# Performance work log

Measured on AMD Instinct MI355X. Metric: run time of the kernel, lower is better.

The kernel has to match this reference:

```python
import jax, jax.numpy as jnp
import numpy as np

N_CLASS = 100
DECAY = 0.3
THRESHOLD = 0.9


def _weighted_centroid(feature, y, prev_centroid):
    # labels/logits from per-class scores
    labels = jnp.argmax(y, axis=1)                      # [n] int
    logits = jnp.max(y, axis=1)                         # [n]
    # per-class counts, clamped at 1
    counts = jax.ops.segment_sum(jnp.ones_like(logits), labels, num_segments=N_CLASS)
    counts = jnp.maximum(counts, 1.0)                   # [n_class]
    # threshold-masked confidence weights
    w = jnp.where(logits > THRESHOLD, logits, 0.0)      # [n]
    # confidence-weighted scatter-add of features by class label
    sums = jax.ops.segment_sum(w[:, None] * feature, labels, num_segments=N_CLASS)  # [n_class, d]
    cur = sums / counts[:, None]
    return (1.0 - DECAY) * prev_centroid + DECAY * cur


def setup_inputs() -> dict:
    key = jax.random.key(0)
    ks = jax.random.split(key, 6)
    n, d = 131072, 256
    return {
        "s_feature": jax.random.normal(ks[0], (n, d), dtype=jnp.float32),
        "t_feature": jax.random.normal(ks[1], (n, d), dtype=jnp.float32),
        "y_s": jax.random.normal(ks[2], (n, N_CLASS), dtype=jnp.float32),
        "y_t": jax.random.normal(ks[3], (n, N_CLASS), dtype=jnp.float32),
        "s_centroid": jax.random.normal(ks[4], (N_CLASS, d), dtype=jnp.float32),
        "t_centroid": jax.random.normal(ks[5], (N_CLASS, d), dtype=jnp.float32),
    }


def reference(s_feature, t_feature, y_s, y_t, s_centroid, t_centroid):
    s_c = _weighted_centroid(s_feature, y_s, s_centroid)
    t_c = _weighted_centroid(t_feature, y_t, t_centroid)
    # MSELoss: mean over all elements
    semantic_loss = jnp.mean((s_c - t_c) ** 2)
    return semantic_loss
```

## Files before the change

### kernel.cpp

```cpp
#include <hip/hip_runtime.h>

#define N_CLASS 100
#define D 256
#define DECAYF 0.3f
#define KEEPF 0.7f
#define THRESH 0.9f
#define RB 64
#define BB 256
#define NSLICE 8

__global__ void argmax_kernel(const float* __restrict__ yS, const float* __restrict__ yT,
                              int* __restrict__ lbl, float* __restrict__ w,
                              int* __restrict__ cntPart, int n, int NB) {
    const int t = blockIdx.y;
    const float* __restrict__ y = t ? yT : yS;

    __shared__ float ly[RB * N_CLASS];
    __shared__ int hist[N_CLASS];
    const int tid = threadIdx.x;
    if (tid < N_CLASS) hist[tid] = 0;

    const float4* __restrict__ src = (const float4*)(y + (size_t)blockIdx.x * (RB * N_CLASS));
    for (int i = tid; i < RB * N_CLASS / 4; i += 256)
        ((float4*)ly)[i] = src[i];
    __syncthreads();

    const int row = tid >> 2;
    const int q = tid & 3;
    const int base = row * N_CLASS + q * 25;

    float best = -3.4e38f;
    int bi = 0;
    #pragma unroll
    for (int k = 0; k < 25; ++k) {
        float v = ly[base + k];
        if (v > best) { best = v; bi = q * 25 + k; }
    }
    #pragma unroll
    for (int off = 1; off <= 2; off <<= 1) {
        float ov = __shfl_xor(best, off, 64);
        int   oi = __shfl_xor(bi, off, 64);
        if (ov > best || (ov == best && oi < bi)) { best = ov; bi = oi; }
    }
    if (q == 0) {
        const int grow = blockIdx.x * RB + row;
        lbl[(size_t)t * n + grow] = bi;
        w[(size_t)t * n + grow] = (best > THRESH) ? best : 0.0f;
        atomicAdd(&hist[bi], 1);
    }
    __syncthreads();
    if (tid < N_CLASS) cntPart[(t * N_CLASS + tid) * NB + blockIdx.x] = hist[tid];
}

__global__ void scan_kernel(const int* __restrict__ cntPart, int* __restrict__ relOff,
                            int* __restrict__ totals, int NB) {
    const int tc = blockIdx.x;
    const int* __restrict__ src = cntPart + (size_t)tc * NB;
    int* __restrict__ dst = relOff + (size_t)tc * NB;
    const int tid = threadIdx.x;
    const int EPT = NB / 256;

    int v[8];
    int s = 0;
    for (int k = 0; k < EPT; ++k) { v[k] = src[tid * EPT + k]; s += v[k]; }

    __shared__ int ls[256];
    ls[tid] = s;
    __syncthreads();
    for (int off = 1; off < 256; off <<= 1) {
        int x = (tid >= off) ? ls[tid - off] : 0;
        __syncthreads();
        ls[tid] += x;
        __syncthreads();
    }
    int run = (tid ? ls[tid - 1] : 0);
    for (int k = 0; k < EPT; ++k) { dst[tid * EPT + k] = run; run += v[k]; }
    if (tid == 255) totals[tc] = run;
}

__global__ void base_kernel(const int* __restrict__ totals, int* __restrict__ classBase) {
    __shared__ int ls[2][128];
    const int t = threadIdx.x >> 7;
    const int c = threadIdx.x & 127;
    int v = (c < N_CLASS) ? totals[t * N_CLASS + c] : 0;
    ls[t][c] = v;
    __syncthreads();
    for (int off = 1; off < 128; off <<= 1) {
        int x = (c >= off) ? ls[t][c - off] : 0;
        __syncthreads();
        ls[t][c] += x;
        __syncthreads();
    }
    if (c < N_CLASS) classBase[t * N_CLASS + c] = ls[t][c] - v;
}

__global__ void bucket_kernel(const int* __restrict__ lbl, const float* __restrict__ w,
                              const int* __restrict__ relOff, const int* __restrict__ classBase,
                              int2* __restrict__ sPair, int n, int NB) {
    const int t = blockIdx.y;
    const int b = blockIdx.x;
    __shared__ int cursor[N_CLASS];
    const int tid = threadIdx.x;
    if (tid < N_CLASS)
        cursor[tid] = classBase[t * N_CLASS + tid] +
                      relOff[(size_t)(t * N_CLASS + tid) * NB + 4 * b];
    __syncthreads();
    const int row = b * BB + tid;
    const int l = lbl[(size_t)t * n + row];
    const float wt = w[(size_t)t * n + row];
    const int pos = atomicAdd(&cursor[l], 1);
    sPair[(size_t)t * n + pos] = make_int2(row, __float_as_int(wt));
}

__global__ void __launch_bounds__(256, 4)
gather_kernel(const float* __restrict__ fS, const float* __restrict__ fT,
              const int2* __restrict__ sPair,
              const int* __restrict__ totals, const int* __restrict__ classBase,
              float* __restrict__ partial, int n) {
    const int c = blockIdx.x;
    const int s = blockIdx.y;
    const int t = blockIdx.z;
    const float* __restrict__ f = t ? fT : fS;
    const int2* __restrict__ sp = sPair + (size_t)t * n;

    const int start = classBase[t * N_CLASS + c];
    const int cnt = totals[t * N_CLASS + c];
    const int per = (cnt + NSLICE - 1) / NSLICE;
    int lo = start + s * per;
    int hi = start + cnt;
    if (lo + per < hi) hi = lo + per;
    if (hi < lo) hi = lo;

    const int tid = threadIdx.x;
    const int lane = tid & 63;
    const int wv = tid >> 6;

    float4 acc = {0.f, 0.f, 0.f, 0.f};
    const int span = hi - lo;
    const int m = span / 32;

    int2 p[8];
    if (m > 0) {
        const int i0 = lo + wv * 8;
        #pragma unroll
        for (int j = 0; j < 8; ++j) p[j] = sp[i0 + j];
    }
    for (int kk = 0; kk < m; ++kk) {
        float4 v[8];
        #pragma unroll
        for (int j = 0; j < 8; ++j)
            v[j] = *(const float4*)(f + (size_t)p[j].x * D + lane * 4);
        int2 np[8];
        if (kk + 1 < m) {
            const int i1 = lo + (kk + 1) * 32 + wv * 8;
            #pragma unroll
            for (int j = 0; j < 8; ++j) np[j] = sp[i1 + j];
        }
        #pragma unroll
        for (int j = 0; j < 8; ++j) {
            const float wt = __int_as_float(p[j].y);
            acc.x += wt * v[j].x; acc.y += wt * v[j].y;
            acc.z += wt * v[j].z; acc.w += wt * v[j].w;
        }
        #pragma unroll
        for (int j = 0; j < 8; ++j) p[j] = np[j];
    }
    for (int r = lo + m * 32 + wv; r < hi; r += 4) {
        const int2 pr = sp[r];
        const float wt = __int_as_float(pr.y);
        const float4 v = *(const float4*)(f + (size_t)pr.x * D + lane * 4);
        acc.x += wt * v.x; acc.y += wt * v.y; acc.z += wt * v.z; acc.w += wt * v.w;
    }

    __shared__ float4 red[4][64];
    red[wv][lane] = acc;
    __syncthreads();
    if (wv == 0) {
        float4 a0 = red[0][lane], a1 = red[1][lane], a2 = red[2][lane], a3 = red[3][lane];
        float4 r4;
        r4.x = a0.x + a1.x + a2.x + a3.x;
        r4.y = a0.y + a1.y + a2.y + a3.y;
        r4.z = a0.z + a1.z + a2.z + a3.z;
        r4.w = a0.w + a1.w + a2.w + a3.w;
        *(float4*)(partial + (size_t)((t * N_CLASS + c) * NSLICE + s) * D + lane * 4) = r4;
    }
}

__global__ void finalize_kernel(const float* __restrict__ partial, const int* __restrict__ totals,
                                const float* __restrict__ cS, const float* __restrict__ cT,
                                float* __restrict__ out) {
    const int c = blockIdx.x;
    const int j = threadIdx.x;

    float sS = 0.f, sT = 0.f;
    #pragma unroll
    for (int s = 0; s < NSLICE; ++s) {
        sS += partial[(size_t)((0 * N_CLASS + c) * NSLICE + s) * D + j];
        sT += partial[(size_t)((1 * N_CLASS + c) * NSLICE + s) * D + j];
    }
    const float cntS = fmaxf((float)totals[c], 1.0f);
    const float cntT = fmaxf((float)totals[N_CLASS + c], 1.0f);
    const float a = KEEPF * cS[c * D + j] + DECAYF * sS / cntS;
    const float b = KEEPF * cT[c * D + j] + DECAYF * sT / cntT;
    const float d = a - b;
    float val = d * d;

    #pragma unroll
    for (int off = 32; off; off >>= 1) val += __shfl_xor(val, off, 64);
    __shared__ float red[4];
    if ((j & 63) == 0) red[j >> 6] = val;
    __syncthreads();
    if (j == 0)
        unsafeAtomicAdd(out, (red[0] + red[1] + red[2] + red[3]) * (1.0f / (N_CLASS * D)));
}

extern "C" void kernel_launch(void* const* d_in, const int* in_sizes, int n_in,
                              void* d_out, int out_size, void* d_ws, size_t ws_size,
                              hipStream_t stream) {
    const float* s_feature = (const float*)d_in[0];
    const float* t_feature = (const float*)d_in[1];
    const float* y_s = (const float*)d_in[2];
    const float* y_t = (const float*)d_in[3];
    const float* s_centroid = (const float*)d_in[4];
    const float* t_centroid = (const float*)d_in[5];
    float* out = (float*)d_out;

    const int n = in_sizes[0] / D;
    const int NB = n / RB;

    int* lbl = (int*)d_ws;
    float* w = (float*)(lbl + 2 * n);
    int* cntPart = (int*)(w + 2 * n);
    int* relOff = cntPart + 2 * N_CLASS * NB;
    int* totals = relOff + 2 * N_CLASS * NB;
    int* classBase = totals + 256;
    int2* sPair = (int2*)(classBase + 256);
    float* partial = (float*)(sPair + 2 * n);

    hipMemsetAsync(out, 0, sizeof(float), stream);

    argmax_kernel<<<dim3(NB, 2), 256, 0, stream>>>(y_s, y_t, lbl, w, cntPart, n, NB);
    scan_kernel<<<2 * N_CLASS, 256, 0, stream>>>(cntPart, relOff, totals, NB);
    base_kernel<<<1, 256, 0, stream>>>(totals, classBase);
    bucket_kernel<<<dim3(n / BB, 2), BB, 0, stream>>>(lbl, w, relOff, classBase, sPair, n, NB);
    gather_kernel<<<dim3(N_CLASS, NSLICE, 2), 256, 0, stream>>>(s_feature, t_feature, sPair,
                                                                totals, classBase, partial, n);
    finalize_kernel<<<N_CLASS, 256, 0, stream>>>(partial, totals, s_centroid, t_centroid, out);
}
```

Before: 369.6 us.

## Fuse argmax and class scatter into one kernel with LDS atomic accumulation

Replaces the six-kernel pipeline (argmax, count scan, base offsets, bucket sort, gather, finalize) with two kernels. In the new main kernel each wave reads one row's scores and features per step, prefetching the next row, and finds the argmax with wave shuffles. It then atomically adds the weighted features into a per-block 100x256 accumulator held in shared memory. A second kernel sums the per-block partials, applies the centroid update and reduces the MSE. This drops the intermediate label and pair arrays, the scans and the scattered gather, reading each input once and streaming. The costs are LDS atomic contention, 100KB of shared memory per block that limits occupancy, and extra partial-buffer traffic for the cross-block reduction.

Result: slower. 626.6 us (+69.5%).

```diff
diff --git a/kernel.cpp b/kernel.cpp
--- a/kernel.cpp
+++ b/kernel.cpp
@@ -5,213 +5,126 @@
 #define DECAYF 0.3f
 #define KEEPF 0.7f
 #define THRESH 0.9f
-#define RB 64
-#define BB 256
-#define NSLICE 8
+#define ACC_SZ (N_CLASS * D)
 
-__global__ void argmax_kernel(const float* __restrict__ yS, const float* __restrict__ yT,
-                              int* __restrict__ lbl, float* __restrict__ w,
-                              int* __restrict__ cntPart, int n, int NB) {
+__global__ void __launch_bounds__(1024)
+mega_kernel(const float* __restrict__ fS, const float* __restrict__ fT,
+            const float* __restrict__ yS, const float* __restrict__ yT,
+            float* __restrict__ partial, int* __restrict__ counts,
+            int n, int B) {
     const int t = blockIdx.y;
+    const float* __restrict__ f = t ? fT : fS;
     const float* __restrict__ y = t ? yT : yS;
 
-    __shared__ float ly[RB * N_CLASS];
-    __shared__ int hist[N_CLASS];
+    __shared__ __align__(16) float acc[ACC_SZ];
+    __shared__ int cnt[N_CLASS];
+
     const int tid = threadIdx.x;
-    if (tid < N_CLASS) hist[tid] = 0;
-
-    const float4* __restrict__ src = (const float4*)(y + (size_t)blockIdx.x * (RB * N_CLASS));
-    for (int i = tid; i < RB * N_CLASS / 4; i += 256)
-        ((float4*)ly)[i] = src[i];
+    for (int i = tid; i < ACC_SZ; i += 1024) acc[i] = 0.f;
+    if (tid < N_CLASS) cnt[tid] = 0;
     __syncthreads();
 
-    const int row = tid >> 2;
-    const int q = tid & 3;
-    const int base = row * N_CLASS + q * 25;
+    const int lane = tid & 63;
+    const int wv = tid >> 6;
+    const int RPB = n / B;
+    const int RPW = RPB >> 4;
+    const int base = blockIdx.x * RPB + wv * RPW;
 
-    float best = -3.4e38f;
-    int bi = 0;
-    #pragma unroll
-    for (int k = 0; k < 25; ++k) {
-        float v = ly[base + k];
-        if (v > best) { best = v; bi = q * 25 + k; }
+    float4 yq = make_float4(0.f, 0.f, 0.f, 0.f);
+    if (lane < N_CLASS / 4)
+        yq = ((const float4*)(y + (size_t)base * N_CLASS))[lane];
+    float4 fv = *(const float4*)(f + (size_t)base * D + lane * 4);
+
+    for (int i = 0; i < RPW; ++i) {
+        float4 nyq = make_float4(0.f, 0.f, 0.f, 0.f);
+        float4 nfv = make_float4(0.f, 0.f, 0.f, 0.f);
+        if (i + 1 < RPW) {
+            const int nrow = base + i + 1;
+            if (lane < N_CLASS / 4)
+                nyq = ((const float4*)(y + (size_t)nrow * N_CLASS))[lane];
+            nfv = *(const float4*)(f + (size_t)nrow * D + lane * 4);
+        }
+
+        float best = -3.4e38f;
+        int bi = 0x7fffffff;
+        if (lane < N_CLASS / 4) {
+            const int c0 = lane * 4;
+            if (yq.x > best) { best = yq.x; bi = c0;     }
+            if (yq.y > best) { best = yq.y; bi = c0 + 1; }
+            if (yq.z > best) { best = yq.z; bi = c0 + 2; }
+            if (yq.w > best) { best = yq.w; bi = c0 + 3; }
+        }
+        #pragma unroll
+        for (int off = 1; off < 64; off <<= 1) {
+            const float ov = __shfl_xor(best, off, 64);
+            const int   oi = __shfl_xor(bi, off, 64);
+            if (ov > best || (ov == best && oi < bi)) { best = ov; bi = oi; }
+        }
+        const float wt = (best > THRESH) ? best : 0.f;
+        if (lane == 0) atomicAdd(&cnt[bi], 1);
+
+        float* a = acc + bi * D + lane;
+        atomicAdd(a,       wt * fv.x);
+        atomicAdd(a + 64,  wt * fv.y);
+        atomicAdd(a + 128, wt * fv.z);
+        atomicAdd(a + 192, wt * fv.w);
+
+        yq = nyq; fv = nfv;
+    }
+    __syncthreads();
+
+    float* outP = partial + ((size_t)t * B + blockIdx.x) * ACC_SZ;
+    for (int i = tid; i < ACC_SZ / 4; i += 1024)
+        ((float4*)outP)[i] = ((const float4*)acc)[i];
+    if (tid < N_CLASS) atomicAdd(&counts[t * N_CLASS + tid], cnt[tid]);
+}
+
+__global__ void __launch_bounds__(512)
+reduce_kernel(const float* __restrict__ partial, const int* __restrict__ counts,
+              const float* __restrict__ cS, const float* __restrict__ cT,
+              float* __restrict__ out, int B) {
+    const int c = blockIdx.x;
+    const int tid = threadIdx.x;
+    const int t = tid >> 8;
+    const int j = tid & 255;
+
+    const float* __restrict__ p = partial + (size_t)t * B * ACC_SZ + c * D + j;
+    float s = 0.f;
+    int b = 0;
+    for (; b + 4 <= B; b += 4) {
+        const float a0 = p[(size_t)(b + 0) * ACC_SZ];
+        const float a1 = p[(size_t)(b + 1) * ACC_SZ];
+        const float a2 = p[(size_t)(b + 2) * ACC_SZ];
+        const float a3 = p[(size_t)(b + 3) * ACC_SZ];
+        s += a0 + a1 + a2 + a3;
+    }
+    for (; b < B; ++b) s += p[(size_t)b * ACC_SZ];
+
+    const float cf = fmaxf((float)counts[t * N_CLASS + c], 1.0f);
+    const int c_log = 4 * (j & 63) + (j >> 6);
+    const float* __restrict__ cX = t ? cT : cS;
+    const float upd = KEEPF * cX[c * D + c_log] + DECAYF * s / cf;
+
+    __shared__ float u[2][D];
+    u[t][j] = upd;
+    __syncthreads();
+
+    float val = 0.f;
+    if (t == 0) {
+        const float d = u[0][j] - u[1][j];
+        val = d * d;
     }
     #pragma unroll
-    for (int off = 1; off <= 2; off <<= 1) {
-        float ov = __shfl_xor(best, off, 64);
-        int   oi = __shfl_xor(bi, off, 64);
-        if (ov > best || (ov == best && oi < bi)) { best = ov; bi = oi; }
+    for (int off = 32; off; off >>= 1) val += __shfl_xor(val, off, 64);
+    __shared__ float red[8];
+    if ((tid & 63) == 0) red[tid >> 6] = val;
+    __syncthreads();
+    if (tid == 0) {
+        float tot = 0.f;
+        #pragma unroll
+        for (int k = 0; k < 8; ++k) tot += red[k];
+        unsafeAtomicAdd(out, tot * (1.0f / (N_CLASS * D)));
     }
-    if (q == 0) {
-        const int grow = blockIdx.x * RB + row;
-        lbl[(size_t)t * n + grow] = bi;
-        w[(size_t)t * n + grow] = (best > THRESH) ? best : 0.0f;
-        atomicAdd(&hist[bi], 1);
-    }
-    __syncthreads();
-    if (tid < N_CLASS) cntPart[(t * N_CLASS + tid) * NB + blockIdx.x] = hist[tid];
-}
-
-__global__ void scan_kernel(const int* __restrict__ cntPart, int* __restrict__ relOff,
-                            int* __restrict__ totals, int NB) {
-    const int tc = blockIdx.x;
-    const int* __restrict__ src = cntPart + (size_t)tc * NB;
-    int* __restrict__ dst = relOff + (size_t)tc * NB;
-    const int tid = threadIdx.x;
-    const int EPT = NB / 256;
-
-    int v[8];
-    int s = 0;
-    for (int k = 0; k < EPT; ++k) { v[k] = src[tid * EPT + k]; s += v[k]; }
-
-    __shared__ int ls[256];
-    ls[tid] = s;
-    __syncthreads();
-    for (int off = 1; off < 256; off <<= 1) {
-        int x = (tid >= off) ? ls[tid - off] : 0;
-        __syncthreads();
-        ls[tid] += x;
-        __syncthreads();
-    }
-    int run = (tid ? ls[tid - 1] : 0);
-    for (int k = 0; k < EPT; ++k) { dst[tid * EPT + k] = run; run += v[k]; }
-    if (tid == 255) totals[tc] = run;
-}
-
-__global__ void base_kernel(const int* __restrict__ totals, int* __restrict__ classBase) {
-    __shared__ int ls[2][128];
-    const int t = threadIdx.x >> 7;
-    const int c = threadIdx.x & 127;
-    int v = (c < N_CLASS) ? totals[t * N_CLASS + c] : 0;
-    ls[t][c] = v;
-    __syncthreads();
-    for (int off = 1; off < 128; off <<= 1) {
-        int x = (c >= off) ? ls[t][c - off] : 0;
-        __syncthreads();
-        ls[t][c] += x;
-        __syncthreads();
-    }
-    if (c < N_CLASS) classBase[t * N_CLASS + c] = ls[t][c] - v;
-}
-
-__global__ void bucket_kernel(const int* __restrict__ lbl, const float* __restrict__ w,
-                              const int* __restrict__ relOff, const int* __restrict__ classBase,
-                              int2* __restrict__ sPair, int n, int NB) {
-    const int t = blockIdx.y;
-    const int b = blockIdx.x;
-    __shared__ int cursor[N_CLASS];
-    const int tid = threadIdx.x;
-    if (tid < N_CLASS)
-        cursor[tid] = classBase[t * N_CLASS + tid] +
-                      relOff[(size_t)(t * N_CLASS + tid) * NB + 4 * b];
-    __syncthreads();
-    const int row = b * BB + tid;
-    const int l = lbl[(size_t)t * n + row];
-    const float wt = w[(size_t)t * n + row];
-    const int pos = atomicAdd(&cursor[l], 1);
-    sPair[(size_t)t * n + pos] = make_int2(row, __float_as_int(wt));
-}
-
-__global__ void __launch_bounds__(256, 4)
-gather_kernel(const float* __restrict__ fS, const float* __restrict__ fT,
-              const int2* __restrict__ sPair,
-              const int* __restrict__ totals, const int* __restrict__ classBase,
-              float* __restrict__ partial, int n) {
-    const int c = blockIdx.x;
-    const int s = blockIdx.y;
-    const int t = blockIdx.z;
-    const float* __restrict__ f = t ? fT : fS;
-    const int2* __restrict__ sp = sPair + (size_t)t * n;
-
-    const int start = classBase[t * N_CLASS + c];
-    const int cnt = totals[t * N_CLASS + c];
-    const int per = (cnt + NSLICE - 1) / NSLICE;
-    int lo = start + s * per;
-    int hi = start + cnt;
-    if (lo + per < hi) hi = lo + per;
-    if (hi < lo) hi = lo;
-
-    const int tid = threadIdx.x;
-    const int lane = tid & 63;
-    const int wv = tid >> 6;
-
-    float4 acc = {0.f, 0.f, 0.f, 0.f};
-    const int span = hi - lo;
-    const int m = span / 32;
-
-    int2 p[8];
-    if (m > 0) {
-        const int i0 = lo + wv * 8;
-        #pragma unroll
-        for (int j = 0; j < 8; ++j) p[j] = sp[i0 + j];
-    }
-    for (int kk = 0; kk < m; ++kk) {
-        float4 v[8];
-        #pragma unroll
-        for (int j = 0; j < 8; ++j)
-            v[j] = *(const float4*)(f + (size_t)p[j].x * D + lane * 4);
-        int2 np[8];
-        if (kk + 1 < m) {
-            const int i1 = lo + (kk + 1) * 32 + wv * 8;
-            #pragma unroll
-            for (int j = 0; j < 8; ++j) np[j] = sp[i1 + j];
-        }
-        #pragma unroll
-        for (int j = 0; j < 8; ++j) {
-            const float wt = __int_as_float(p[j].y);
-            acc.x += wt * v[j].x; acc.y += wt * v[j].y;
-            acc.z += wt * v[j].z; acc.w += wt * v[j].w;
-        }
-        #pragma unroll
-        for (int j = 0; j < 8; ++j) p[j] = np[j];
-    }
-    for (int r = lo + m * 32 + wv; r < hi; r += 4) {
-        const int2 pr = sp[r];
-        const float wt = __int_as_float(pr.y);
-        const float4 v = *(const float4*)(f + (size_t)pr.x * D + lane * 4);
-        acc.x += wt * v.x; acc.y += wt * v.y; acc.z += wt * v.z; acc.w += wt * v.w;
-    }
-
-    __shared__ float4 red[4][64];
-    red[wv][lane] = acc;
-    __syncthreads();
-    if (wv == 0) {
-        float4 a0 = red[0][lane], a1 = red[1][lane], a2 = red[2][lane], a3 = red[3][lane];
-        float4 r4;
-        r4.x = a0.x + a1.x + a2.x + a3.x;
-        r4.y = a0.y + a1.y + a2.y + a3.y;
-        r4.z = a0.z + a1.z + a2.z + a3.z;
-        r4.w = a0.w + a1.w + a2.w + a3.w;
-        *(float4*)(partial + (size_t)((t * N_CLASS + c) * NSLICE + s) * D + lane * 4) = r4;
-    }
-}
-
-__global__ void finalize_kernel(const float* __restrict__ partial, const int* __restrict__ totals,
-                                const float* __restrict__ cS, const float* __restrict__ cT,
-                                float* __restrict__ out) {
-    const int c = blockIdx.x;
-    const int j = threadIdx.x;
-
-    float sS = 0.f, sT = 0.f;
-    #pragma unroll
-    for (int s = 0; s < NSLICE; ++s) {
-        sS += partial[(size_t)((0 * N_CLASS + c) * NSLICE + s) * D + j];
-        sT += partial[(size_t)((1 * N_CLASS + c) * NSLICE + s) * D + j];
-    }
-    const float cntS = fmaxf((float)totals[c], 1.0f);
-    const float cntT = fmaxf((float)totals[N_CLASS + c], 1.0f);
-    const float a = KEEPF * cS[c * D + j] + DECAYF * sS / cntS;
-    const float b = KEEPF * cT[c * D + j] + DECAYF * sT / cntT;
-    const float d = a - b;
-    float val = d * d;
-
-    #pragma unroll
-    for (int off = 32; off; off >>= 1) val += __shfl_xor(val, off, 64);
-    __shared__ float red[4];
-    if ((j & 63) == 0) red[j >> 6] = val;
-    __syncthreads();
-    if (j == 0)
-        unsafeAtomicAdd(out, (red[0] + red[1] + red[2] + red[3]) * (1.0f / (N_CLASS * D)));
 }
 
 extern "C" void kernel_launch(void* const* d_in, const int* in_sizes, int n_in,
@@ -226,24 +139,18 @@
     float* out = (float*)d_out;
 
     const int n = in_sizes[0] / D;
-    const int NB = n / RB;
 
-    int* lbl = (int*)d_ws;
-    float* w = (float*)(lbl + 2 * n);
-    int* cntPart = (int*)(w + 2 * n);
-    int* relOff = cntPart + 2 * N_CLASS * NB;
-    int* totals = relOff + 2 * N_CLASS * NB;
-    int* classBase = totals + 256;
-    int2* sPair = (int2*)(classBase + 256);
-    float* partial = (float*)(sPair + 2 * n);
+    int B = 128;
+    while (B > 8 && (size_t)2 * B * ACC_SZ * sizeof(float) + 1024 > ws_size) B >>= 1;
+
+    float* partial = (float*)d_ws;
+    int* counts = (int*)(partial + (size_t)2 * B * ACC_SZ);
 
     hipMemsetAsync(out, 0, sizeof(float), stream);
+    hipMemsetAsync(counts, 0, 256 * sizeof(int), stream);
 
-    argmax_kernel<<<dim3(NB, 2), 256, 0, stream>>>(y_s, y_t, lbl, w, cntPart, n, NB);
-    scan_kernel<<<2 * N_CLASS, 256, 0, stream>>>(cntPart, relOff, totals, NB);
-    base_kernel<<<1, 256, 0, stream>>>(totals, classBase);
-    bucket_kernel<<<dim3(n / BB, 2), BB, 0, stream>>>(lbl, w, relOff, classBase, sPair, n, NB);
-    gather_kernel<<<dim3(N_CLASS, NSLICE, 2), 256, 0, stream>>>(s_feature, t_feature, sPair,
-                                                                totals, classBase, partial, n);
-    finalize_kernel<<<N_CLASS, 256, 0, stream>>>(partial, totals, s_centroid, t_centroid, out);
+    mega_kernel<<<dim3(B, 2), 1024, 0, stream>>>(s_feature, t_feature, y_s, y_t,
+                                                 partial, counts, n, B);
+    reduce_kernel<<<N_CLASS, 512, 0, stream>>>(partial, counts,
+                                               s_centroid, t_centroid, out, B);
 }
```
